# Performance work log

Measured on AMD Instinct MI355X. Metric: run time of the kernel, lower is better.

Reference implementation:

```python
import jax, jax.numpy as jnp
import numpy as np

N = 100000   # num nodes
E = 1600000  # num edges
D = 128      # input_dim
K = 5        # APPNP propagation steps
EPS = 1e-8   # torch cosine_similarity eps


def setup_inputs() -> dict:
    key = jax.random.key(0)
    k1, k2, k3, k4 = jax.random.split(key, 4)
    x = jax.random.normal(k1, (N, D), jnp.float32)
    mask = jax.random.normal(k2, (N, 1), jnp.float32)
    edge_index = jax.random.randint(k3, (2, E), 0, N, dtype=jnp.int32)
    # init_t: orthogonal weight with gain sqrt(2), zero bias
    W = jax.nn.initializers.orthogonal(scale=2 ** 0.5)(k4, (D, D), jnp.float32)
    b = jnp.zeros((D,), jnp.float32)
    alpha = jnp.array(0.5, jnp.float32)
    return {"x": x, "mask": mask, "edge_index": edge_index, "W": W, "b": b, "alpha": alpha}


def reference(x, mask, edge_index, W, b, alpha):
    n = x.shape[0]
    # x_fn: Linear + Tanh
    h = jnp.tanh(x @ W.T + b)
    src, dst = edge_index[0], edge_index[1]
    hs, hd = h[src], h[dst]  # [E, D] gathers
    # torch F.cosine_similarity with eps-clamped norms
    dot = jnp.sum(hs * hd, axis=-1)
    ns = jnp.maximum(jnp.sqrt(jnp.sum(hs * hs, axis=-1)), EPS)
    nd = jnp.maximum(jnp.sqrt(jnp.sum(hd * hd, axis=-1)), EPS)
    edge_weights = jax.nn.relu(dot / (ns * nd))  # [E]

    fill = jax.nn.relu(mask)  # [N, 1]

    # PyG APPNP: gcn_norm with self loops (fill value 1.0)
    loops = jnp.arange(n, dtype=src.dtype)
    row = jnp.concatenate([src, loops])
    col = jnp.concatenate([dst, loops])
    w = jnp.concatenate([edge_weights, jnp.ones((n,), edge_weights.dtype)])
    deg = jax.ops.segment_sum(w, col, num_segments=n)
    dinv = jnp.where(deg > 0, jax.lax.rsqrt(jnp.maximum(deg, EPS)), 0.0)
    norm = dinv[row] * w * dinv[col]  # [E+N]

    # K-step APPNP: z <- (1-alpha) * A_hat z + alpha * fill
    z = fill
    for _ in range(K):
        agg = jax.ops.segment_sum(norm[:, None] * z[row], col, num_segments=n)
        z = (1.0 - alpha) * agg + alpha * fill
    return z, edge_weights
```

## Files before the change

### kernel.cpp

```cpp
#include <hip/hip_runtime.h>
#include <hip/hip_bf16.h>

typedef __attribute__((ext_vector_type(2))) float f32x2;
typedef __attribute__((ext_vector_type(4))) float f32x4;
typedef __attribute__((ext_vector_type(8))) short short8;

#define D 128
#define EPS 1e-8f
#define BSH 8
#define BSZ 256
#define SMAX 8000
#define OSH 12
#define OBK 4096

__device__ __forceinline__ short f2bf(float f) {
    unsigned int u = __float_as_uint(f);
    unsigned int r = (u + 0x7fffu + ((u >> 16) & 1u)) >> 16;
    return (short)r;
}

__device__ __forceinline__ unsigned int pkbf(float lo, float hi) {
    unsigned int r;
    asm("v_cvt_pk_bf16_f32 %0, %1, %2" : "=v"(r) : "v"(lo), "v"(hi));
    return r;
}

__device__ __forceinline__ float ftanh(float y) {
    float e = __builtin_amdgcn_exp2f(y * 2.885390082f);
    float r = __builtin_amdgcn_rcpf(e + 1.0f);
    return __builtin_fmaf(-2.0f, r, 1.0f);
}

__device__ __forceinline__ int dot4(unsigned int a, unsigned int b, int c) {
#if __has_builtin(__builtin_amdgcn_sdot4)
    return __builtin_amdgcn_sdot4((int)a, (int)b, c, false);
#else
    int r = c;
    r += (int)(char)(a) * (int)(char)(b);
    r += (int)(char)(a >> 8) * (int)(char)(b >> 8);
    r += (int)(char)(a >> 16) * (int)(char)(b >> 16);
    r += (int)(char)(a >> 24) * (int)(char)(b >> 24);
    return r;
#endif
}

__global__ __launch_bounds__(256) void cvinit_kernel(const float* __restrict__ W,
                                                     short* __restrict__ Wbf,
                                                     const float* __restrict__ mask,
                                                     float* __restrict__ fill, int N) {
    int i = blockIdx.x * 256 + threadIdx.x;
    if (i < N) fill[i] = fmaxf(mask[i], 0.0f);
    if (i < D * D) Wbf[i] = f2bf(W[i]);
}

__global__ __launch_bounds__(256) void gemm_kernel(const float* __restrict__ x,
                                                   const short* __restrict__ Wbf,
                                                   const float* __restrict__ b,
                                                   signed char* __restrict__ hn8,
                                                   int N) {
    __shared__ char Wlds[D * D * 2];
    int tid  = threadIdx.x;
    {
        const uint4* ws = (const uint4*)Wbf;
#pragma unroll
        for (int c = 0; c < 8; ++c) {
            int i = c * 256 + tid;
            int byte = i << 4;
            int swz  = byte ^ (((byte >> 8) & 15) << 4);
            *(uint4*)(Wlds + swz) = ws[i];
        }
    }
    __syncthreads();

    int wave = tid >> 6;
    int lane = tid & 63;
    int l16  = lane & 15;
    int g    = lane >> 4;
    int r0   = blockIdx.x * 64 + wave * 16;

    int arow = r0 + l16;
    if (arow >= N) arow = N - 1;
    union { uint4 u; short8 s; } afr[4];
    const float* xp = x + (size_t)arow * D + g * 8;
#pragma unroll
    for (int kc = 0; kc < 4; ++kc) {
        float4 lo = *(const float4*)(xp + kc * 32);
        float4 hi = *(const float4*)(xp + kc * 32 + 4);
        afr[kc].u.x = pkbf(lo.x, lo.y);
        afr[kc].u.y = pkbf(lo.z, lo.w);
        afr[kc].u.z = pkbf(hi.x, hi.y);
        afr[kc].u.w = pkbf(hi.z, hi.w);
    }

    float bj[8];
#pragma unroll
    for (int j = 0; j < 8; ++j) bj[j] = b[j * 16 + l16];

    f32x4 acc[8];
#pragma unroll
    for (int j = 0; j < 8; ++j) acc[j] = (f32x4){0.f, 0.f, 0.f, 0.f};

#pragma unroll
    for (int j = 0; j < 8; ++j) {
#pragma unroll
        for (int kc = 0; kc < 4; ++kc) {
            int addr = (j * 16 + l16) * 256 + kc * 64 + g * 16;
            const short8* bp = (const short8*)(Wlds + (addr ^ (l16 << 4)));
            acc[j] = __builtin_amdgcn_mfma_f32_16x16x32_bf16(afr[kc].s, *bp, acc[j], 0, 0, 0);
        }
    }

    float sq[4] = {0.f, 0.f, 0.f, 0.f};
#pragma unroll
    for (int j = 0; j < 8; ++j) {
#pragma unroll
        for (int r = 0; r < 4; ++r) {
            float tt = ftanh(acc[j][r] + bj[j]);
            acc[j][r] = tt;
            sq[r] = __builtin_fmaf(tt, tt, sq[r]);
        }
    }
#pragma unroll
    for (int m = 1; m <= 8; m <<= 1) {
#pragma unroll
        for (int r = 0; r < 4; ++r) sq[r] += __shfl_xor(sq[r], m);
    }
#pragma unroll
    for (int r = 0; r < 4; ++r) {
        float inv = rsqrtf(fmaxf(sq[r], 1e-16f)) * 127.0f;
        int row = r0 + g * 4 + r;
        if (row < N) {
#pragma unroll
            for (int j = 0; j < 8; ++j) {
                hn8[(size_t)row * D + j * 16 + l16] =
                    (signed char)__float2int_rn(acc[j][r] * inv);
            }
        }
    }
}

__global__ __launch_bounds__(256) void bcnt_kernel(const int* __restrict__ dst,
                                                   int* __restrict__ M,
                                                   int E, int nbk, int nblk, int chunk) {
    extern __shared__ int cnt[];
    int b = blockIdx.x;
    for (int k = threadIdx.x; k < nbk; k += 256) cnt[k] = 0;
    __syncthreads();
    int beg = b * chunk, end = min(E, beg + chunk);
    for (int e = beg + threadIdx.x; e < end; e += 256)
        atomicAdd(&cnt[dst[e] >> BSH], 1);
    __syncthreads();
    for (int k = threadIdx.x; k < nbk; k += 256)
        M[k * nblk + b] = cnt[k];
}

__global__ __launch_bounds__(1024) void scan_blk(const int* __restrict__ cnt,
                                                 int* __restrict__ rp,
                                                 int* __restrict__ bsum, int nq) {
    __shared__ int wsum[16];
    __shared__ int sexcl[16];
    int tid = threadIdx.x, lane = tid & 63, wv = tid >> 6;
    int idx = blockIdx.x * 1024 + tid;
    int4 c = (idx < nq) ? ((const int4*)cnt)[idx] : make_int4(0, 0, 0, 0);
    int tsum = c.x + c.y + c.z + c.w;
    int incl = tsum;
#pragma unroll
    for (int m = 1; m < 64; m <<= 1) {
        int t = __shfl_up(incl, m);
        if (lane >= m) incl += t;
    }
    if (lane == 63) wsum[wv] = incl;
    __syncthreads();
    if (tid == 0) {
        int acc = 0;
#pragma unroll
        for (int k = 0; k < 16; ++k) { int t = wsum[k]; sexcl[k] = acc; acc += t; }
        bsum[blockIdx.x] = acc;
    }
    __syncthreads();
    int excl = sexcl[wv] + incl - tsum;
    if (idx < nq) {
        int4 r;
        r.x = excl; r.y = excl + c.x; r.z = r.y + c.y; r.w = r.z + c.z;
        ((int4*)rp)[idx] = r;
    }
}

__global__ __launch_bounds__(256) void scan_top(int* __restrict__ bsum,
                                                int* __restrict__ boff, int nbs,
                                                int* __restrict__ gcur, int nbk2) {
    for (int k = threadIdx.x; k < nbk2; k += 256) gcur[k] = k << OSH;
    if (threadIdx.x == 0) {
        int acc = 0;
        for (int k = 0; k < nbs; ++k) { int t = bsum[k]; boff[k] = acc; acc += t; }
    }
}

__global__ __launch_bounds__(256) void scan_add(int* __restrict__ data,
                                                const int* __restrict__ boff, int nq) {
    int idx = blockIdx.x * 256 + threadIdx.x;
    if (idx < nq) {
        int off = boff[idx >> 10];
        int4 r = ((int4*)data)[idx];
        r.x += off; r.y += off; r.z += off; r.w += off;
        ((int4*)data)[idx] = r;
    }
}

__global__ __launch_bounds__(256) void bscat_kernel(const int* __restrict__ src,
                                                    const int* __restrict__ dst,
                                                    const int* __restrict__ Mo,
                                                    int2* __restrict__ ebuf,
                                                    int E, int nbk, int nblk, int chunk) {
    extern __shared__ int cur[];
    int b = blockIdx.x;
    for (int k = threadIdx.x; k < nbk; k += 256) cur[k] = Mo[k * nblk + b];
    __syncthreads();
    int beg = b * chunk, end = min(E, beg + chunk);
    for (int e = beg + threadIdx.x; e < end; e += 256) {
        int d = dst[e];
        int k = d >> BSH;
        int p = atomicAdd(&cur[k], 1);
        ebuf[p] = make_int2(src[e], (e << BSH) | (d & (BSZ - 1)));
    }
}

__global__ __launch_bounds__(256) void binsort_kernel(const int* __restrict__ Mo,
                                                      const int2* __restrict__ ebuf,
                                                      int* __restrict__ esrc,
                                                      int* __restrict__ eorig,
                                                      int* __restrict__ rp,
                                                      int E, int N, int nbk, int nblk) {
    extern __shared__ char smem[];
    int2* stage = (int2*)smem;
    int*  cnt   = (int*)(smem + SMAX * 8);
    int k = blockIdx.x;
    int base = Mo[k * nblk];
    int endb = (k + 1 < nbk) ? Mo[(k + 1) * nblk] : E;
    int m = endb - base;
    if (m > SMAX) m = SMAX;

    if (threadIdx.x < BSZ) cnt[threadIdx.x] = 0;
    __syncthreads();
    for (int i = threadIdx.x; i < m; i += 256) {
        int2 v = ebuf[base + i];
        stage[i] = v;
        atomicAdd(&cnt[v.y & (BSZ - 1)], 1);
    }
    __syncthreads();
    if (threadIdx.x == 0) {
        int acc = 0;
#pragma unroll 8
        for (int t = 0; t < BSZ; ++t) { int c = cnt[t]; cnt[t] = acc; acc += c; }
    }
    __syncthreads();
    {
        int node = (k << BSH) + threadIdx.x;
        if (threadIdx.x < BSZ && node < N) rp[node] = base + cnt[threadIdx.x];
        if (k == nbk - 1 && threadIdx.x == 0) rp[N] = E;
    }
    __syncthreads();
    for (int i = threadIdx.x; i < m; i += 256) {
        int2 v = stage[i];
        int p = atomicAdd(&cnt[v.y & (BSZ - 1)], 1);
        esrc[base + p]  = v.x;
        eorig[base + p] = v.y >> BSH;
    }
}

__global__ __launch_bounds__(256) void weight_kernel(const int* __restrict__ rp,
                                                     const int* __restrict__ esrc,
                                                     const signed char* __restrict__ hn8,
                                                     float* __restrict__ warr,
                                                     float* __restrict__ deg, int N) {
    const float SC = 1.0f / 16129.0f;
    int gid = (blockIdx.x * 256 + threadIdx.x) >> 3;
    int l   = threadIdx.x & 7;
    if (gid >= N) return;
    const uint4* hp = (const uint4*)hn8;
    uint4 dv = hp[(size_t)gid * 8 + l];
    int beg = rp[gid], end = rp[gid + 1];
    float sum = 0.f;
    int s = beg;
    for (; s + 3 < end; s += 4) {
        int i0 = esrc[s], i1 = esrc[s + 1], i2 = esrc[s + 2], i3 = esrc[s + 3];
        uint4 u0 = hp[(size_t)i0 * 8 + l];
        uint4 u1 = hp[(size_t)i1 * 8 + l];
        uint4 u2 = hp[(size_t)i2 * 8 + l];
        uint4 u3 = hp[(size_t)i3 * 8 + l];
        int d0 = dot4(u0.x, dv.x, 0); d0 = dot4(u0.y, dv.y, d0);
        d0 = dot4(u0.z, dv.z, d0);    d0 = dot4(u0.w, dv.w, d0);
        int d1 = dot4(u1.x, dv.x, 0); d1 = dot4(u1.y, dv.y, d1);
        d1 = dot4(u1.z, dv.z, d1);    d1 = dot4(u1.w, dv.w, d1);
        int d2 = dot4(u2.x, dv.x, 0); d2 = dot4(u2.y, dv.y, d2);
        d2 = dot4(u2.z, dv.z, d2);    d2 = dot4(u2.w, dv.w, d2);
        int d3 = dot4(u3.x, dv.x, 0); d3 = dot4(u3.y, dv.y, d3);
        d3 = dot4(u3.z, dv.z, d3);    d3 = dot4(u3.w, dv.w, d3);
#pragma unroll
        for (int m = 4; m >= 1; m >>= 1) {
            d0 += __shfl_xor(d0, m); d1 += __shfl_xor(d1, m);
            d2 += __shfl_xor(d2, m); d3 += __shfl_xor(d3, m);
        }
        float w0 = fmaxf((float)d0 * SC, 0.f), w1 = fmaxf((float)d1 * SC, 0.f);
        float w2 = fmaxf((float)d2 * SC, 0.f), w3 = fmaxf((float)d3 * SC, 0.f);
        if (l == 0) { warr[s] = w0; warr[s + 1] = w1; warr[s + 2] = w2; warr[s + 3] = w3; }
        sum += (w0 + w1) + (w2 + w3);
    }
    for (; s < end; ++s) {
        int i0 = esrc[s];
        uint4 u0 = hp[(size_t)i0 * 8 + l];
        int d0 = dot4(u0.x, dv.x, 0); d0 = dot4(u0.y, dv.y, d0);
        d0 = dot4(u0.z, dv.z, d0);    d0 = dot4(u0.w, dv.w, d0);
#pragma unroll
        for (int m = 4; m >= 1; m >>= 1) d0 += __shfl_xor(d0, m);
        float w0 = fmaxf((float)d0 * SC, 0.f);
        if (l == 0) warr[s] = w0;
        sum += w0;
    }
    if (l == 0) deg[gid] = 1.0f + sum;
}

__global__ __launch_bounds__(256) void dscat_kernel(const int* __restrict__ eorig,
                                                    const float* __restrict__ warr,
                                                    int* __restrict__ gcur,
                                                    int2* __restrict__ pbuf,
                                                    int E, int nbk2, int chunk) {
    extern __shared__ char smem[];
    int2* stage = (int2*)smem;
    int*  hist  = (int*)(smem + (size_t)chunk * 8);
    int*  lcur  = hist + nbk2;
    int b = blockIdx.x;
    for (int k = threadIdx.x; k < nbk2; k += 256) hist[k] = 0;
    __syncthreads();
    int beg = b * chunk, end = min(E, beg + chunk), m = end - beg;
    for (int i = threadIdx.x; i < m; i += 256) {
        int o = eorig[beg + i];
        float w = warr[beg + i];
        stage[i] = make_int2(o, __float_as_int(w));
        atomicAdd(&hist[o >> OSH], 1);
    }
    __syncthreads();
    for (int k = threadIdx.x; k < nbk2; k += 256) {
        int c = hist[k];
        lcur[k] = c ? atomicAdd(&gcur[k], c) : 0;
    }
    __syncthreads();
    for (int i = threadIdx.x; i < m; i += 256) {
        int2 v = stage[i];
        int p = atomicAdd(&lcur[v.x >> OSH], 1);
        pbuf[p] = v;
    }
}

__global__ __launch_bounds__(256) void dfin_kernel(const int2* __restrict__ pbuf,
                                                   float* __restrict__ ew, int E,
                                                   const float* __restrict__ deg,
                                                   float* __restrict__ dinv, int N) {
    int i = blockIdx.x * 256 + threadIdx.x;
    if (i < N) {
        float dg = deg[i];
        dinv[i] = (dg > 0.f) ? rsqrtf(fmaxf(dg, EPS)) : 0.f;
    }
    int base = blockIdx.x << OSH;
    int m = min(OBK, E - base);
    for (int t = threadIdx.x; t < m; t += 256) {
        int2 v = pbuf[base + t];
        ew[v.x] = __int_as_float(v.y);
    }
}

__global__ __launch_bounds__(256) void appnp_first_kernel(const int* __restrict__ rp,
                                                          const int* __restrict__ esrc,
                                                          const float* __restrict__ warr,
                                                          float* __restrict__ wfin,
                                                          const float* __restrict__ dinv,
                                                          const float* __restrict__ fill,
                                                          const float* __restrict__ alpha,
                                                          float* __restrict__ zout, int N) {
    int t = blockIdx.x * 256 + threadIdx.x;
    int i = t >> 2, l = t & 3;
    if (i >= N) return;
    int beg = rp[i], end = rp[i + 1];
    float al = alpha[0];
    float oma = 1.0f - al;
    float di = dinv[i];
    float s = 0.f;
    for (int j = beg + l; j < end; j += 4) {
        int sr = esrc[j];
        float wf = oma * warr[j] * di * dinv[sr];
        wfin[j] = wf;
        s += wf * fill[sr];
    }
    s += __shfl_xor(s, 1);
    s += __shfl_xor(s, 2);
    if (l == 0) {
        float fi = fill[i];
        zout[i] = al * fi + oma * di * di * fi + s;
    }
}

__global__ __launch_bounds__(256) void appnp_kernel(const int* __restrict__ rp,
                                                    const int* __restrict__ esrc,
                                                    const float* __restrict__ wfin,
                                                    const float* __restrict__ dinv,
                                                    const float* __restrict__ fill,
                                                    const float* __restrict__ zin,
                                                    const float* __restrict__ alpha,
                                                    float* __restrict__ zout, int N) {
    int t = blockIdx.x * 256 + threadIdx.x;
    int i = t >> 2, l = t & 3;
    if (i >= N) return;
    int beg = rp[i], end = rp[i + 1];
    float s = 0.f;
    for (int j = beg + l; j < end; j += 4)
        s += wfin[j] * zin[esrc[j]];
    s += __shfl_xor(s, 1);
    s += __shfl_xor(s, 2);
    if (l == 0) {
        float al = alpha[0];
        float di = dinv[i];
        zout[i] = al * fill[i] + (1.0f - al) * di * di * zin[i] + s;
    }
}

extern "C" void kernel_launch(void* const* d_in, const int* in_sizes, int n_in,
                              void* d_out, int out_size, void* d_ws, size_t ws_size,
                              hipStream_t stream) {
    const float* x     = (const float*)d_in[0];
    const float* mask  = (const float*)d_in[1];
    const int*   ei    = (const int*)d_in[2];
    const float* W     = (const float*)d_in[3];
    const float* b     = (const float*)d_in[4];
    const float* alpha = (const float*)d_in[5];

    int N = in_sizes[1];
    int E = in_sizes[2] / 2;
    const int* src = ei;
    const int* dst = ei + E;

    float* out = (float*)d_out;
    float* ew  = out + N;

    int Np = (N + 15) & ~15;

    int NBK  = (N + BSZ - 1) >> BSH;
    int NBLK = 400;
    int CHUNK = (E + NBLK - 1) / NBLK;
    int L = NBK * NBLK;

    int NBK2   = (E + OBK - 1) >> OSH;
    int NBLK2  = 400;
    int CHUNK2 = (E + NBLK2 - 1) / NBLK2;

    char* wsb = (char*)d_ws;
    signed char* hn8 = (signed char*)wsb;
    int2* pbuf = (int2*)wsb;
    char* p = wsb + (size_t)N * D;
    short* Wbf  = (short*)p;           p += (size_t)D * D * 2;
    float* deg  = (float*)p;           p += (size_t)Np * 4;
    float* dinv = (float*)p;           p += (size_t)Np * 4;
    float* fill = (float*)p;           p += (size_t)Np * 4;
    float* zA   = (float*)p;           p += (size_t)Np * 4;
    float* zB   = (float*)p;           p += (size_t)Np * 4;
    int*   rp   = (int*)p;             p += (size_t)(Np + 16) * 4;
    int*   M    = (int*)p;             p += (size_t)L * 4;
    int*   Mo   = (int*)p;             p += (size_t)(L + 16) * 4;
    int*   bsum = (int*)p;             p += 64 * 4;
    int*   boff = (int*)p;             p += 64 * 4;
    int*   gcur = (int*)p;             p += 512 * 4;
    int2*  ebuf = (int2*)p;            p += (size_t)E * 8;
    int*   esrc = (int*)p;             p += (size_t)E * 4;
    int*   eorig= (int*)p;             p += (size_t)E * 4;
    float* warr = (float*)p;
    float* wfin = (float*)eorig;

    int nb_n = (N + 255) / 256;
    int nb_n4 = ((size_t)N * 4 + 255) / 256;
    int nq   = L / 4;
    int nbs  = (nq + 1023) / 1024;
    int ldsA = ((NBK * 4) + 15) & ~15;
    int ldsB = SMAX * 8 + BSZ * 4;
    int ldsD = CHUNK2 * 8 + 2 * NBK2 * 4;

    cvinit_kernel<<<nb_n, 256, 0, stream>>>(W, Wbf, mask, fill, N);
    gemm_kernel<<<(N + 63) / 64, 256, 0, stream>>>(x, Wbf, b, hn8, N);

    bcnt_kernel<<<NBLK, 256, ldsA, stream>>>(dst, M, E, NBK, NBLK, CHUNK);
    scan_blk<<<nbs, 1024, 0, stream>>>(M, Mo, bsum, nq);
    scan_top<<<1, 256, 0, stream>>>(bsum, boff, nbs, gcur, NBK2);
    scan_add<<<(nq + 255) / 256, 256, 0, stream>>>(Mo, boff, nq);
    bscat_kernel<<<NBLK, 256, ldsA, stream>>>(src, dst, Mo, ebuf, E, NBK, NBLK, CHUNK);
    binsort_kernel<<<NBK, 256, ldsB, stream>>>(Mo, ebuf, esrc, eorig, rp, E, N, NBK, NBLK);

    weight_kernel<<<((size_t)N * 8 + 255) / 256, 256, 0, stream>>>(rp, esrc, hn8, warr, deg, N);

    dscat_kernel<<<NBLK2, 256, ldsD, stream>>>(eorig, warr, gcur, pbuf, E, NBK2, CHUNK2);
    dfin_kernel<<<NBK2, 256, 0, stream>>>(pbuf, ew, E, deg, dinv, N);

    appnp_first_kernel<<<nb_n4, 256, 0, stream>>>(rp, esrc, warr, wfin, dinv, fill, alpha, zA, N);
    appnp_kernel<<<nb_n4, 256, 0, stream>>>(rp, esrc, wfin, dinv, fill, zA, alpha, zB, N);
    appnp_kernel<<<nb_n4, 256, 0, stream>>>(rp, esrc, wfin, dinv, fill, zB, alpha, zA, N);
    appnp_kernel<<<nb_n4, 256, 0, stream>>>(rp, esrc, wfin, dinv, fill, zA, alpha, zB, N);
    appnp_kernel<<<nb_n4, 256, 0, stream>>>(rp, esrc, wfin, dinv, fill, zB, alpha, out, N);
}
```

Before: 219.1 us.

## Merge independent kernels into horizontally fused launches to cut launch count

Folds the W-to-bf16 conversion into the GEMM prologue. The GEMM, fill computation and bucket counting now share one launch, split by block index. The dscatter pass is merged with the first APPNP step, and the edge-weight writeback (dfin) with the second. dinv is computed directly in weight_kernel, which removes the deg buffer, and wfin gets its own buffer instead of aliasing eorig. This cuts about four kernel launches and their serialization gaps. The cost is heterogeneous blocks in each launch, and the dscat blocks carry the larger LDS allocation into the APPNP blocks, which may reduce occupancy.

```diff
diff --git a/kernel.cpp b/kernel.cpp
--- a/kernel.cpp
+++ b/kernel.cpp
@@ -12,12 +12,6 @@
 #define SMAX 8000
 #define OSH 12
 #define OBK 4096
-
-__device__ __forceinline__ short f2bf(float f) {
-    unsigned int u = __float_as_uint(f);
-    unsigned int r = (u + 0x7fffu + ((u >> 16) & 1u)) >> 16;
-    return (short)r;
-}
 
 __device__ __forceinline__ unsigned int pkbf(float lo, float hi) {
     unsigned int r;
@@ -44,31 +38,47 @@
 #endif
 }
 
-__global__ __launch_bounds__(256) void cvinit_kernel(const float* __restrict__ W,
-                                                     short* __restrict__ Wbf,
-                                                     const float* __restrict__ mask,
-                                                     float* __restrict__ fill, int N) {
-    int i = blockIdx.x * 256 + threadIdx.x;
-    if (i < N) fill[i] = fmaxf(mask[i], 0.0f);
-    if (i < D * D) Wbf[i] = f2bf(W[i]);
-}
-
-__global__ __launch_bounds__(256) void gemm_kernel(const float* __restrict__ x,
-                                                   const short* __restrict__ Wbf,
+__global__ __launch_bounds__(256) void k1_gemm_aux(const float* __restrict__ x,
+                                                   const float* __restrict__ W,
                                                    const float* __restrict__ b,
                                                    signed char* __restrict__ hn8,
-                                                   int N) {
+                                                   int N,
+                                                   const float* __restrict__ mask,
+                                                   float* __restrict__ fill,
+                                                   const int* __restrict__ dst,
+                                                   int* __restrict__ M,
+                                                   int E, int nbk, int nblk, int chunk,
+                                                   int gemmNB) {
     __shared__ char Wlds[D * D * 2];
-    int tid  = threadIdx.x;
-    {
-        const uint4* ws = (const uint4*)Wbf;
-#pragma unroll
-        for (int c = 0; c < 8; ++c) {
-            int i = c * 256 + tid;
-            int byte = i << 4;
-            int swz  = byte ^ (((byte >> 8) & 15) << 4);
-            *(uint4*)(Wlds + swz) = ws[i];
-        }
+    int tid = threadIdx.x;
+
+    if (blockIdx.x >= gemmNB) {
+        int baux = blockIdx.x - gemmNB;
+        int* cnt = (int*)Wlds;
+        for (int k = tid; k < nbk; k += 256) cnt[k] = 0;
+        int fi = baux * 256 + tid;
+        if (fi < N) fill[fi] = fmaxf(mask[fi], 0.0f);
+        __syncthreads();
+        int beg = baux * chunk, end = min(E, beg + chunk);
+        for (int e = beg + tid; e < end; e += 256)
+            atomicAdd(&cnt[dst[e] >> BSH], 1);
+        __syncthreads();
+        for (int k = tid; k < nbk; k += 256)
+            M[k * nblk + baux] = cnt[k];
+        return;
+    }
+
+#pragma unroll
+    for (int c = 0; c < 8; ++c) {
+        int i = c * 256 + tid;
+        float4 lo = *(const float4*)(W + i * 8);
+        float4 hi = *(const float4*)(W + i * 8 + 4);
+        uint4 v;
+        v.x = pkbf(lo.x, lo.y); v.y = pkbf(lo.z, lo.w);
+        v.z = pkbf(hi.x, hi.y); v.w = pkbf(hi.z, hi.w);
+        int byte = i << 4;
+        int swz  = byte ^ (((byte >> 8) & 15) << 4);
+        *(uint4*)(Wlds + swz) = v;
     }
     __syncthreads();
 
@@ -137,21 +147,6 @@
             }
         }
     }
-}
-
-__global__ __launch_bounds__(256) void bcnt_kernel(const int* __restrict__ dst,
-                                                   int* __restrict__ M,
-                                                   int E, int nbk, int nblk, int chunk) {
-    extern __shared__ int cnt[];
-    int b = blockIdx.x;
-    for (int k = threadIdx.x; k < nbk; k += 256) cnt[k] = 0;
-    __syncthreads();
-    int beg = b * chunk, end = min(E, beg + chunk);
-    for (int e = beg + threadIdx.x; e < end; e += 256)
-        atomicAdd(&cnt[dst[e] >> BSH], 1);
-    __syncthreads();
-    for (int k = threadIdx.x; k < nbk; k += 256)
-        M[k * nblk + b] = cnt[k];
 }
 
 __global__ __launch_bounds__(1024) void scan_blk(const int* __restrict__ cnt,
@@ -272,7 +267,7 @@
                                                      const int* __restrict__ esrc,
                                                      const signed char* __restrict__ hn8,
                                                      float* __restrict__ warr,
-                                                     float* __restrict__ deg, int N) {
+                                                     float* __restrict__ dinv, int N) {
     const float SC = 1.0f / 16129.0f;
     int gid = (blockIdx.x * 256 + threadIdx.x) >> 3;
     int l   = threadIdx.x & 7;
@@ -317,67 +312,51 @@
         if (l == 0) warr[s] = w0;
         sum += w0;
     }
-    if (l == 0) deg[gid] = 1.0f + sum;
-}
-
-__global__ __launch_bounds__(256) void dscat_kernel(const int* __restrict__ eorig,
-                                                    const float* __restrict__ warr,
-                                                    int* __restrict__ gcur,
-                                                    int2* __restrict__ pbuf,
-                                                    int E, int nbk2, int chunk) {
-    extern __shared__ char smem[];
-    int2* stage = (int2*)smem;
-    int*  hist  = (int*)(smem + (size_t)chunk * 8);
-    int*  lcur  = hist + nbk2;
-    int b = blockIdx.x;
-    for (int k = threadIdx.x; k < nbk2; k += 256) hist[k] = 0;
-    __syncthreads();
-    int beg = b * chunk, end = min(E, beg + chunk), m = end - beg;
-    for (int i = threadIdx.x; i < m; i += 256) {
-        int o = eorig[beg + i];
-        float w = warr[beg + i];
-        stage[i] = make_int2(o, __float_as_int(w));
-        atomicAdd(&hist[o >> OSH], 1);
-    }
-    __syncthreads();
-    for (int k = threadIdx.x; k < nbk2; k += 256) {
-        int c = hist[k];
-        lcur[k] = c ? atomicAdd(&gcur[k], c) : 0;
-    }
-    __syncthreads();
-    for (int i = threadIdx.x; i < m; i += 256) {
-        int2 v = stage[i];
-        int p = atomicAdd(&lcur[v.x >> OSH], 1);
-        pbuf[p] = v;
-    }
-}
-
-__global__ __launch_bounds__(256) void dfin_kernel(const int2* __restrict__ pbuf,
-                                                   float* __restrict__ ew, int E,
-                                                   const float* __restrict__ deg,
-                                                   float* __restrict__ dinv, int N) {
-    int i = blockIdx.x * 256 + threadIdx.x;
-    if (i < N) {
-        float dg = deg[i];
-        dinv[i] = (dg > 0.f) ? rsqrtf(fmaxf(dg, EPS)) : 0.f;
-    }
-    int base = blockIdx.x << OSH;
-    int m = min(OBK, E - base);
-    for (int t = threadIdx.x; t < m; t += 256) {
-        int2 v = pbuf[base + t];
-        ew[v.x] = __int_as_float(v.y);
-    }
-}
-
-__global__ __launch_bounds__(256) void appnp_first_kernel(const int* __restrict__ rp,
-                                                          const int* __restrict__ esrc,
-                                                          const float* __restrict__ warr,
-                                                          float* __restrict__ wfin,
-                                                          const float* __restrict__ dinv,
-                                                          const float* __restrict__ fill,
-                                                          const float* __restrict__ alpha,
-                                                          float* __restrict__ zout, int N) {
-    int t = blockIdx.x * 256 + threadIdx.x;
+    if (l == 0) dinv[gid] = rsqrtf(1.0f + sum);
+}
+
+__global__ __launch_bounds__(256) void k6_dscat_appnp1(const int* __restrict__ eorig,
+                                                       const float* __restrict__ warr,
+                                                       int* __restrict__ gcur,
+                                                       int2* __restrict__ pbuf,
+                                                       int E, int nbk2, int chunk,
+                                                       int dscatNB,
+                                                       const int* __restrict__ rp,
+                                                       const int* __restrict__ esrc,
+                                                       float* __restrict__ wfin,
+                                                       const float* __restrict__ dinv,
+                                                       const float* __restrict__ fill,
+                                                       const float* __restrict__ alpha,
+                                                       float* __restrict__ zout, int N) {
+    if (blockIdx.x < dscatNB) {
+        extern __shared__ char smem[];
+        int2* stage = (int2*)smem;
+        int*  hist  = (int*)(smem + (size_t)chunk * 8);
+        int*  lcur  = hist + nbk2;
+        int b = blockIdx.x;
+        for (int k = threadIdx.x; k < nbk2; k += 256) hist[k] = 0;
+        __syncthreads();
+        int beg = b * chunk, end = min(E, beg + chunk), m = end - beg;
+        for (int i = threadIdx.x; i < m; i += 256) {
+            int o = eorig[beg + i];
+            float w = warr[beg + i];
+            stage[i] = make_int2(o, __float_as_int(w));
+            atomicAdd(&hist[o >> OSH], 1);
+        }
+        __syncthreads();
+        for (int k = threadIdx.x; k < nbk2; k += 256) {
+            int c = hist[k];
+            lcur[k] = c ? atomicAdd(&gcur[k], c) : 0;
+        }
+        __syncthreads();
+        for (int i = threadIdx.x; i < m; i += 256) {
+            int2 v = stage[i];
+            int p = atomicAdd(&lcur[v.x >> OSH], 1);
+            pbuf[p] = v;
+        }
+        return;
+    }
+    int t = (blockIdx.x - dscatNB) * 256 + threadIdx.x;
     int i = t >> 2, l = t & 3;
     if (i >= N) return;
     int beg = rp[i], end = rp[i + 1];
@@ -396,6 +375,43 @@
     if (l == 0) {
         float fi = fill[i];
         zout[i] = al * fi + oma * di * di * fi + s;
+    }
+}
+
+__global__ __launch_bounds__(256) void k7_appnp2_dfin(const int* __restrict__ rp,
+                                                      const int* __restrict__ esrc,
+                                                      const float* __restrict__ wfin,
+                                                      const float* __restrict__ dinv,
+                                                      const float* __restrict__ fill,
+                                                      const float* __restrict__ zin,
+                                                      const float* __restrict__ alpha,
+                                                      float* __restrict__ zout, int N,
+                                                      int appnpNB,
+                                                      const int2* __restrict__ pbuf,
+                                                      float* __restrict__ ew, int E) {
+    if (blockIdx.x >= appnpNB) {
+        int bk = blockIdx.x - appnpNB;
+        int base = bk << OSH;
+        int m = min(OBK, E - base);
+        for (int t = threadIdx.x; t < m; t += 256) {
+            int2 v = pbuf[base + t];
+            ew[v.x] = __int_as_float(v.y);
+        }
+        return;
+    }
+    int t = blockIdx.x * 256 + threadIdx.x;
+    int i = t >> 2, l = t & 3;
+    if (i >= N) return;
+    int beg = rp[i], end = rp[i + 1];
+    float s = 0.f;
+    for (int j = beg + l; j < end; j += 4)
+        s += wfin[j] * zin[esrc[j]];
+    s += __shfl_xor(s, 1);
+    s += __shfl_xor(s, 2);
+    if (l == 0) {
+        float al = alpha[0];
+        float di = dinv[i];
+        zout[i] = al * fill[i] + (1.0f - al) * di * di * zin[i] + s;
     }
 }
 
@@ -452,12 +468,13 @@
     int NBLK2  = 400;
     int CHUNK2 = (E + NBLK2 - 1) / NBLK2;
 
+    int GEMM_NB = (N + 63) / 64;
+    int nb_n4   = ((size_t)N * 4 + 255) / 256;
+
     char* wsb = (char*)d_ws;
     signed char* hn8 = (signed char*)wsb;
     int2* pbuf = (int2*)wsb;
     char* p = wsb + (size_t)N * D;
-    short* Wbf  = (short*)p;           p += (size_t)D * D * 2;
-    float* deg  = (float*)p;           p += (size_t)Np * 4;
     float* dinv = (float*)p;           p += (size_t)Np * 4;
     float* fill = (float*)p;           p += (size_t)Np * 4;
     float* zA   = (float*)p;           p += (size_t)Np * 4;
@@ -471,34 +488,33 @@
     int2*  ebuf = (int2*)p;            p += (size_t)E * 8;
     int*   esrc = (int*)p;             p += (size_t)E * 4;
     int*   eorig= (int*)p;             p += (size_t)E * 4;
-    float* warr = (float*)p;
-    float* wfin = (float*)eorig;
-
-    int nb_n = (N + 255) / 256;
-    int nb_n4 = ((size_t)N * 4 + 255) / 256;
+    float* warr = (float*)p;           p += (size_t)E * 4;
+    float* wfin = (float*)p;
+
     int nq   = L / 4;
     int nbs  = (nq + 1023) / 1024;
     int ldsA = ((NBK * 4) + 15) & ~15;
     int ldsB = SMAX * 8 + BSZ * 4;
     int ldsD = CHUNK2 * 8 + 2 * NBK2 * 4;
 
-    cvinit_kernel<<<nb_n, 256, 0, stream>>>(W, Wbf, mask, fill, N);
-    gemm_kernel<<<(N + 63) / 64, 256, 0, stream>>>(x, Wbf, b, hn8, N);
-
-    bcnt_kernel<<<NBLK, 256, ldsA, stream>>>(dst, M, E, NBK, NBLK, CHUNK);
+    k1_gemm_aux<<<GEMM_NB + NBLK, 256, 0, stream>>>(x, W, b, hn8, N, mask, fill,
+                                                    dst, M, E, NBK, NBLK, CHUNK, GEMM_NB);
     scan_blk<<<nbs, 1024, 0, stream>>>(M, Mo, bsum, nq);
     scan_top<<<1, 256, 0, stream>>>(bsum, boff, nbs, gcur, NBK2);
     scan_add<<<(nq + 255) / 256, 256, 0, stream>>>(Mo, boff, nq);
     bscat_kernel<<<NBLK, 256, ldsA, stream>>>(src, dst, Mo, ebuf, E, NBK, NBLK, CHUNK);
     binsort_kernel<<<NBK, 256, ldsB, stream>>>(Mo, ebuf, esrc, eorig, rp, E, N, NBK, NBLK);
 
-    weight_kernel<<<((size_t)N * 8 + 255) / 256, 256, 0, stream>>>(rp, esrc, hn8, warr, deg, N);
-
-    dscat_kernel<<<NBLK2, 256, ldsD, stream>>>(eorig, warr, gcur, pbuf, E, NBK2, CHUNK2);
-    dfin_kernel<<<NBK2, 256, 0, stream>>>(pbuf, ew, E, deg, dinv, N);
-
-    appnp_first_kernel<<<nb_n4, 256, 0, stream>>>(rp, esrc, warr, wfin, dinv, fill, alpha, zA, N);
-    appnp_kernel<<<nb_n4, 256, 0, stream>>>(rp, esrc, wfin, dinv, fill, zA, alpha, zB, N);
+    weight_kernel<<<((size_t)N * 8 + 255) / 256, 256, 0, stream>>>(rp, esrc, hn8, warr, dinv, N);
+
+    k6_dscat_appnp1<<<NBLK2 + nb_n4, 256, ldsD, stream>>>(eorig, warr, gcur, pbuf,
+                                                          E, NBK2, CHUNK2, NBLK2,
+                                                          rp, esrc, wfin, dinv, fill,
+                                                          alpha, zA, N);
+    k7_appnp2_dfin<<<nb_n4 + NBK2, 256, 0, stream>>>(rp, esrc, wfin, dinv, fill,
+                                                     zA, alpha, zB, N, nb_n4,
+                                                     pbuf, ew, E);
+
     appnp_kernel<<<nb_n4, 256, 0, stream>>>(rp, esrc, wfin, dinv, fill, zB, alpha, zA, N);
     appnp_kernel<<<nb_n4, 256, 0, stream>>>(rp, esrc, wfin, dinv, fill, zA, alpha, zB, N);
     appnp_kernel<<<nb_n4, 256, 0, stream>>>(rp, esrc, wfin, dinv, fill, zB, alpha, out, N);
```

Result: faster. 199.8 us (-8.8%).
